# Optimization experiments

Measured on AMD Instinct MI355X. Metric: run time of the kernel, lower is better.

## Reference

```python
import jax, jax.numpy as jnp
import numpy as np

T, B, H = 2048, 32, 1024
L1, L2, L3 = 100, 10, 1  # cascade 100 -> 10 -> 1 from linear_size=100


def setup_inputs() -> dict:
    key = jax.random.key(0)
    ks = jax.random.split(key, 8)
    def lin_init(k, fan_in, shape):
        # torch nn.Linear default: U(-1/sqrt(fan_in), 1/sqrt(fan_in))
        bound = 1.0 / np.sqrt(fan_in)
        return jax.random.uniform(k, shape, jnp.float32, -bound, bound)
    return {
        "encoder_output": jax.random.normal(ks[0], (T, B, H), jnp.float32),
        "lengths": jax.random.randint(ks[1], (B,), 1, T + 1, jnp.int64),
        "W1": lin_init(ks[2], H, (L1, H)),
        "b1": lin_init(ks[3], H, (L1,)),
        "W2": lin_init(ks[4], L1, (L2, L1)),
        "b2": lin_init(ks[5], L1, (L2,)),
        "W3": lin_init(ks[6], L2, (L3, L2)),
        "b3": lin_init(ks[7], L2, (L3,)),
    }


def reference(encoder_output, lengths, W1, b1, W2, b2, W3, b3):
    # MLP cascade over all timesteps/batch at once: [T,B,H] -> [T,B,1]
    h = jax.nn.relu(jnp.einsum("tbh,lh->tbl", encoder_output, W1) + b1)
    h = jax.nn.relu(jnp.einsum("tbl,ml->tbm", h, W2) + b2)
    logits = jnp.einsum("tbm,om->tbo", h, W3) + b3  # [T,B,1]
    logp = jax.nn.log_sigmoid(logits)[..., 0]       # [T,B]
    # Mask timesteps beyond each sample's length, sum, exponentiate
    mask = jnp.arange(T)[:, None] < lengths[None, :]  # [T,B]
    return jnp.exp(jnp.sum(jnp.where(mask, logp, 0.0), axis=0))  # [B]
```

## Files before the change

kernel.cpp:

```cpp
#include <hip/hip_runtime.h>
#include <hip/hip_bf16.h>
#include <stdint.h>


#define T_DIM 2048
#define B_DIM 32
#define H_DIM 1024
#define L1_DIM 100
#define L2_DIM 10
#define K2_PAD 128
#define NPART 512

#define W1B_ELEMS (112 * 1024)
#define W2B_ELEMS (16 * 128)
#define PART_OFF_BYTES ((W1B_ELEMS + W2B_ELEMS) * 2)

#define CHUNK_BYTES 14336
#define LDSH_OFF    0
#define LDSW2_OFF   34816
#define LDSPART_OFF 39168
#define LDS_TOTAL   39680

typedef float v4f __attribute__((ext_vector_type(4)));
typedef short s8  __attribute__((ext_vector_type(8)));

static __device__ __forceinline__ unsigned short f2bf(float f) {
    unsigned int u = __float_as_uint(f);
    u += 0x7fffu + ((u >> 16) & 1u);
    return (unsigned short)(u >> 16);
}

static __device__ __forceinline__ s8 pack8(float4 a, float4 b) {
    union { s8 v; __hip_bfloat162 h[4]; } u;
    u.h[0] = __float22bfloat162_rn(make_float2(a.x, a.y));
    u.h[1] = __float22bfloat162_rn(make_float2(a.z, a.w));
    u.h[2] = __float22bfloat162_rn(make_float2(b.x, b.y));
    u.h[3] = __float22bfloat162_rn(make_float2(b.z, b.w));
    return u.v;
}

__global__ void convert_weights(const float* __restrict__ W1,
                                const float* __restrict__ W2,
                                unsigned short* __restrict__ wsb) {
    int i = blockIdx.x * 256 + threadIdx.x;
    if (i < W1B_ELEMS) {
        int row = i >> 10, col = i & 1023;
        float v = (row < L1_DIM) ? W1[row * H_DIM + col] : 0.0f;
        wsb[i] = f2bf(v);
    } else {
        int j = i - W1B_ELEMS;
        if (j < W2B_ELEMS) {
            int r = j >> 7, c = j & 127;
            float v = (r < L2_DIM && c < L1_DIM) ? W2[r * L1_DIM + c] : 0.0f;
            wsb[W1B_ELEMS + j] = f2bf(v);
        }
    }
}

__global__ __launch_bounds__(256) void mlp_main(
    const float* __restrict__ enc,
    const int*   __restrict__ lenp,
    const float* __restrict__ b1,
    const float* __restrict__ b2,
    const float* __restrict__ W3,
    const float* __restrict__ b3,
    const unsigned short* __restrict__ w1b,
    const unsigned short* __restrict__ w2b,
    float* __restrict__ partials)
{
    __shared__ __align__(16) unsigned char smem[LDS_TOTAL];

    const int tid  = threadIdx.x;
    const int blk  = blockIdx.x;
    const int lane = tid & 63;
    const int w    = tid >> 6;
    const int m    = lane & 15;
    const int q    = lane >> 4;

    const bool is64 = (lenp[1] == 0);

    int maxlen = 0;
    for (int i = 0; i < B_DIM; ++i) {
        int L = is64 ? lenp[2 * i] : lenp[i];
        maxlen = max(maxlen, L);
    }
    if (4 * blk >= maxlen) {
        if (tid < 32) partials[tid * NPART + blk] = 0.0f;
        return;
    }

    const int t = 4 * blk + w;
    const int len0 = is64 ? lenp[2 * m] : lenp[m];
    const int len1 = is64 ? lenp[2 * (16 + m)] : lenp[16 + m];
    const bool pred0 = (t < len0);
    const bool pred1 = (t < len1);
    const bool waveActive = (t < maxlen);

    {
        unsigned short* ldsW2 = (unsigned short*)(smem + LDSW2_OFF);
        int r = tid >> 4, c = (tid & 15) << 3;
        *(uint4*)(ldsW2 + r * 136 + c) = *(const uint4*)(w2b + r * K2_PAD + c);
    }

    float b1v[7];
#pragma unroll
    for (int nt = 0; nt < 7; ++nt) {
        int n = nt * 16 + m;
        b1v[nt] = (n < L1_DIM) ? b1[n] : 0.0f;
    }
    const float b2v = (m < L2_DIM) ? b2[m] : 0.0f;
    const float w3v = (m < L2_DIM) ? W3[m] : 0.0f;
    const float b3s = b3[0];

    const float* ap0 = enc + (size_t)(blk * 128 + w * 32 + m) * H_DIM + q * 8;
    const float* ap1 = ap0 + 16 * H_DIM;
    const int fragoff = lane * 16;

    v4f acc0[7], acc1[7];
#pragma unroll
    for (int nt = 0; nt < 7; ++nt) { acc0[nt] = (v4f)0.0f; acc1[nt] = (v4f)0.0f; }

#define STAGE(kc, BASE)                                                        \
    {                                                                          \
        _Pragma("unroll")                                                      \
        for (int it = 0; it < 4; ++it) {                                       \
            int j = it * 256 + tid;                                            \
            if (it < 3 || tid < 128) {                                         \
                int rest = j >> 6;                           \
                int ks = (rest >= 7) ? 1 : 0;                                  \
                int nt = rest - ks * 7;                                        \
                const unsigned short* g = w1b + (nt * 16 + (j & 15)) * H_DIM + \
                                          (kc) * 64 + ks * 32 + ((j >> 4) & 3) * 8; \
                __builtin_amdgcn_global_load_lds(                              \
                    (const __attribute__((address_space(1))) unsigned int*)g,  \
                    (__attribute__((address_space(3))) unsigned int*)           \
                        (smem + (BASE) + (j & ~63) * 16),                      \
                    16, 0, 0);                                                 \
            }                                                                  \
        }                                                                      \
    }

#define KBODY(kc, RD, WR)                                                      \
    {                                                                          \
        if ((kc) < 15) STAGE((kc) + 1, WR);                                    \
        if (waveActive) {                                                      \
            const int kb = (kc) * 64;                                          \
            const float4 z4 = make_float4(0.f, 0.f, 0.f, 0.f);                 \
            float4 a00 = pred0 ? *(const float4*)(ap0 + kb)      : z4;         \
            float4 a01 = pred0 ? *(const float4*)(ap0 + kb + 4)  : z4;         \
            float4 a02 = pred0 ? *(const float4*)(ap0 + kb + 32) : z4;         \
            float4 a03 = pred0 ? *(const float4*)(ap0 + kb + 36) : z4;         \
            float4 a10 = pred1 ? *(const float4*)(ap1 + kb)      : z4;         \
            float4 a11 = pred1 ? *(const float4*)(ap1 + kb + 4)  : z4;         \
            float4 a12 = pred1 ? *(const float4*)(ap1 + kb + 32) : z4;         \
            float4 a13 = pred1 ? *(const float4*)(ap1 + kb + 36) : z4;         \
            s8 af0 = pack8(a00, a01);                                          \
            s8 af1 = pack8(a10, a11);                                          \
            _Pragma("unroll")                                                  \
            for (int nt = 0; nt < 7; ++nt) {                                   \
                s8 bf = *(const s8*)(smem + (RD) + nt * 1024 + fragoff);       \
                acc0[nt] = __builtin_amdgcn_mfma_f32_16x16x32_bf16(af0, bf, acc0[nt], 0, 0, 0); \
                acc1[nt] = __builtin_amdgcn_mfma_f32_16x16x32_bf16(af1, bf, acc1[nt], 0, 0, 0); \
            }                                                                  \
            af0 = pack8(a02, a03);                                             \
            af1 = pack8(a12, a13);                                             \
            _Pragma("unroll")                                                  \
            for (int nt = 0; nt < 7; ++nt) {                                   \
                s8 bf = *(const s8*)(smem + (RD) + (7 + nt) * 1024 + fragoff); \
                acc0[nt] = __builtin_amdgcn_mfma_f32_16x16x32_bf16(af0, bf, acc0[nt], 0, 0, 0); \
                acc1[nt] = __builtin_amdgcn_mfma_f32_16x16x32_bf16(af1, bf, acc1[nt], 0, 0, 0); \
            }                                                                  \
        }                                                                      \
        __syncthreads();                                                       \
    }

    STAGE(0, 0)
    __syncthreads();

    KBODY(0, 0, CHUNK_BYTES)
    KBODY(1, CHUNK_BYTES, 0)
    KBODY(2, 0, CHUNK_BYTES)
    KBODY(3, CHUNK_BYTES, 0)
    KBODY(4, 0, CHUNK_BYTES)
    KBODY(5, CHUNK_BYTES, 0)
    KBODY(6, 0, CHUNK_BYTES)
    KBODY(7, CHUNK_BYTES, 0)
    KBODY(8, 0, CHUNK_BYTES)
    KBODY(9, CHUNK_BYTES, 0)
    KBODY(10, 0, CHUNK_BYTES)
    KBODY(11, CHUNK_BYTES, 0)
    KBODY(12, 0, CHUNK_BYTES)
    KBODY(13, CHUNK_BYTES, 0)
    KBODY(14, 0, CHUNK_BYTES)
    KBODY(15, CHUNK_BYTES, 0)

#undef KBODY
#undef STAGE

    unsigned short* ldsH = (unsigned short*)(smem + LDSH_OFF);
#pragma unroll
    for (int f = 0; f < 2; ++f) {
#pragma unroll
        for (int nt = 0; nt < 7; ++nt) {
#pragma unroll
            for (int reg = 0; reg < 4; ++reg) {
                int row = w * 32 + f * 16 + q * 4 + reg;
                int col = nt * 16 + m;
                float a = f ? acc1[nt][reg] : acc0[nt][reg];
                ldsH[row * 136 + col] = f2bf(fmaxf(a + b1v[nt], 0.0f));
            }
        }
    }
    {
        int r = tid >> 1, c = 112 + (tid & 1) * 8;
        uint4 z; z.x = z.y = z.z = z.w = 0u;
        *(uint4*)(ldsH + r * 136 + c) = z;
    }
    __syncthreads();

    unsigned short* ldsW2 = (unsigned short*)(smem + LDSW2_OFF);
    v4f acc2[2];
    acc2[0] = (v4f)0.0f; acc2[1] = (v4f)0.0f;
#pragma unroll
    for (int ks2 = 0; ks2 < 4; ++ks2) {
        s8 bw = *(const s8*)(ldsW2 + m * 136 + ks2 * 32 + q * 8);
#pragma unroll
        for (int f = 0; f < 2; ++f) {
            s8 ah = *(const s8*)(ldsH + (w * 32 + f * 16 + m) * 136 + ks2 * 32 + q * 8);
            acc2[f] = __builtin_amdgcn_mfma_f32_16x16x32_bf16(ah, bw, acc2[f], 0, 0, 0);
        }
    }

    float* ldsPart = (float*)(smem + LDSPART_OFF);
#pragma unroll
    for (int f = 0; f < 2; ++f) {
        v4f zv;
#pragma unroll
        for (int reg = 0; reg < 4; ++reg)
            zv[reg] = fmaxf(acc2[f][reg] + b2v, 0.0f) * w3v;
#pragma unroll
        for (int msk = 1; msk < 16; msk <<= 1) {
#pragma unroll
            for (int reg = 0; reg < 4; ++reg)
                zv[reg] += __shfl_xor(zv[reg], msk, 16);
        }
        if (m == 0) {
#pragma unroll
            for (int reg = 0; reg < 4; ++reg) {
                int b = f * 16 + q * 4 + reg;
                int lenB = is64 ? lenp[2 * b] : lenp[b];
                float logit = zv[reg] + b3s;
                float logp  = fminf(logit, 0.0f) - log1pf(__expf(-fabsf(logit)));
                ldsPart[w * 32 + b] = (t < lenB) ? logp : 0.0f;
            }
        }
    }
    __syncthreads();
    if (tid < 32)
        partials[tid * NPART + blk] =
            (ldsPart[tid] + ldsPart[32 + tid]) + (ldsPart[64 + tid] + ldsPart[96 + tid]);
}

__global__ void finalize(const float* __restrict__ partials,
                         float* __restrict__ out) {
    const int b = blockIdx.x;
    const int tid = threadIdx.x;
    float s = 0.0f;
    for (int i = tid; i < NPART; i += 256) s += partials[b * NPART + i];
#pragma unroll
    for (int off = 32; off > 0; off >>= 1) s += __shfl_down(s, off, 64);
    __shared__ float red[4];
    if ((tid & 63) == 0) red[tid >> 6] = s;
    __syncthreads();
    if (tid == 0) out[b] = expf(red[0] + red[1] + red[2] + red[3]);
}

extern "C" void kernel_launch(void* const* d_in, const int* in_sizes, int n_in,
                              void* d_out, int out_size, void* d_ws, size_t ws_size,
                              hipStream_t stream) {
    const float* enc = (const float*)d_in[0];
    const int*   len = (const int*)d_in[1];
    const float* W1  = (const float*)d_in[2];
    const float* b1  = (const float*)d_in[3];
    const float* W2  = (const float*)d_in[4];
    const float* b2  = (const float*)d_in[5];
    const float* W3  = (const float*)d_in[6];
    const float* b3  = (const float*)d_in[7];

    unsigned short* wsb = (unsigned short*)d_ws;
    float* partials = (float*)((char*)d_ws + PART_OFF_BYTES);
    float* out = (float*)d_out;

    convert_weights<<<(W1B_ELEMS + W2B_ELEMS + 255) / 256, 256, 0, stream>>>(W1, W2, wsb);
    mlp_main<<<NPART, 256, 0, stream>>>(enc, len, b1, b2, W3, b3,
                                        wsb, wsb + W1B_ELEMS, partials);
    finalize<<<B_DIM, 256, 0, stream>>>(partials, out);
}
```

Before: 445.9 us.

## Stage activations through LDS with coalesced loads and pre-swizzle W1 fragments

The encoder activation tile is now loaded cooperatively with row-contiguous, coalesced float4 reads, converted to bf16 and written into a double-buffered LDS region in MFMA fragment order. Previously each wave read A fragments straight from global memory in a strided pattern. W1 is also pre-packed by the conversion kernel into fragment order, so staging becomes one linear copy per chunk, and one barrier before the layer-2 step is removed. This raises LDS use to about 67 KB per block, which may cut occupancy, and adds an LDS write/read round trip for A.

```diff
diff --git a/kernel.cpp b/kernel.cpp
--- a/kernel.cpp
+++ b/kernel.cpp
@@ -3,23 +3,23 @@
 #include <stdint.h>
 
 
-#define T_DIM 2048
-#define B_DIM 32
-#define H_DIM 1024
+#define H_DIM  1024
 #define L1_DIM 100
 #define L2_DIM 10
-#define K2_PAD 128
-#define NPART 512
-
-#define W1B_ELEMS (112 * 1024)
-#define W2B_ELEMS (16 * 128)
-#define PART_OFF_BYTES ((W1B_ELEMS + W2B_ELEMS) * 2)
-
-#define CHUNK_BYTES 14336
-#define LDSH_OFF    0
-#define LDSW2_OFF   34816
-#define LDSPART_OFF 39168
-#define LDS_TOTAL   39680
+#define NPART  512
+
+#define W1P_ELEMS (112 * 1024)
+#define W2P_ELEMS (16 * 128)
+#define PART_OFF_BYTES ((W1P_ELEMS + W2P_ELEMS) * 2)
+
+#define W1CH   14336
+#define ACH    16384
+#define W1_OFF 0
+#define A_OFF  28672
+#define H_OFF  28672
+#define W2_OFF 63488
+#define PRT_OFF 67840
+#define LDS_TOTAL 68352
 
 typedef float v4f __attribute__((ext_vector_type(4)));
 typedef short s8  __attribute__((ext_vector_type(8)));
@@ -42,18 +42,31 @@
 __global__ void convert_weights(const float* __restrict__ W1,
                                 const float* __restrict__ W2,
                                 unsigned short* __restrict__ wsb) {
-    int i = blockIdx.x * 256 + threadIdx.x;
-    if (i < W1B_ELEMS) {
-        int row = i >> 10, col = i & 1023;
-        float v = (row < L1_DIM) ? W1[row * H_DIM + col] : 0.0f;
-        wsb[i] = f2bf(v);
-    } else {
-        int j = i - W1B_ELEMS;
-        if (j < W2B_ELEMS) {
-            int r = j >> 7, c = j & 127;
-            float v = (r < L2_DIM && c < L1_DIM) ? W2[r * L1_DIM + c] : 0.0f;
-            wsb[W1B_ELEMS + j] = f2bf(v);
-        }
+    int s = blockIdx.x * 256 + threadIdx.x;
+    union { uint4 u; unsigned short h[8]; } o;
+    if (s < 14336) {
+        int lane = s & 63, rest = s >> 6;
+        int nt = rest % 7, ksc = rest / 7;
+        int m = lane & 15, q = lane >> 4;
+        int row = nt * 16 + m;
+        int col = ksc * 32 + q * 8;
+        if (row < L1_DIM) {
+            const float* src = W1 + row * H_DIM + col;
+#pragma unroll
+            for (int e = 0; e < 8; ++e) o.h[e] = f2bf(src[e]);
+        } else {
+            o.u = make_uint4(0u, 0u, 0u, 0u);
+        }
+        *(uint4*)(wsb + s * 8) = o.u;
+    } else if (s < 14336 + 256) {
+        int j = s - 14336;
+        int r = j >> 4, c = (j & 15) * 8;
+#pragma unroll
+        for (int e = 0; e < 8; ++e) {
+            int cc = c + e;
+            o.h[e] = (r < L2_DIM && cc < L1_DIM) ? f2bf(W2[r * L1_DIM + cc]) : 0;
+        }
+        *(uint4*)(wsb + W1P_ELEMS + j * 8) = o.u;
     }
 }
 
@@ -64,8 +77,8 @@
     const float* __restrict__ b2,
     const float* __restrict__ W3,
     const float* __restrict__ b3,
-    const unsigned short* __restrict__ w1b,
-    const unsigned short* __restrict__ w2b,
+    const unsigned short* __restrict__ w1p,
+    const unsigned short* __restrict__ w2p,
     float* __restrict__ partials)
 {
     __shared__ __align__(16) unsigned char smem[LDS_TOTAL];
@@ -80,7 +93,7 @@
     const bool is64 = (lenp[1] == 0);
 
     int maxlen = 0;
-    for (int i = 0; i < B_DIM; ++i) {
+    for (int i = 0; i < 32; ++i) {
         int L = is64 ? lenp[2 * i] : lenp[i];
         maxlen = max(maxlen, L);
     }
@@ -89,17 +102,22 @@
         return;
     }
 
+    const int srow = tid >> 3;
+    const int scg  = tid & 7;
+    const int sks  = scg >> 2;
+    const int sq   = scg & 3;
+    const int sf   = srow >> 4;
+    const int sm   = srow & 15;
+    const int sslot = sq * 16 + sm;
+    const int slen = is64 ? lenp[2 * srow] : lenp[srow];
+    const float* sp = enc + ((size_t)(blk * 128) + srow) * H_DIM + scg * 8;
+
     const int t = 4 * blk + w;
-    const int len0 = is64 ? lenp[2 * m] : lenp[m];
-    const int len1 = is64 ? lenp[2 * (16 + m)] : lenp[16 + m];
-    const bool pred0 = (t < len0);
-    const bool pred1 = (t < len1);
     const bool waveActive = (t < maxlen);
 
     {
-        unsigned short* ldsW2 = (unsigned short*)(smem + LDSW2_OFF);
-        int r = tid >> 4, c = (tid & 15) << 3;
-        *(uint4*)(ldsW2 + r * 136 + c) = *(const uint4*)(w2b + r * K2_PAD + c);
+        int r = tid >> 4, c = (tid & 15) * 8;
+        *(uint4*)(smem + W2_OFF + r * 272 + c * 2) = *(const uint4*)(w2p + r * 128 + c);
     }
 
     float b1v[7];
@@ -112,92 +130,107 @@
     const float w3v = (m < L2_DIM) ? W3[m] : 0.0f;
     const float b3s = b3[0];
 
-    const float* ap0 = enc + (size_t)(blk * 128 + w * 32 + m) * H_DIM + q * 8;
-    const float* ap1 = ap0 + 16 * H_DIM;
-    const int fragoff = lane * 16;
-
     v4f acc0[7], acc1[7];
 #pragma unroll
     for (int nt = 0; nt < 7; ++nt) { acc0[nt] = (v4f)0.0f; acc1[nt] = (v4f)0.0f; }
 
-#define STAGE(kc, BASE)                                                        \
-    {                                                                          \
-        _Pragma("unroll")                                                      \
-        for (int it = 0; it < 4; ++it) {                                       \
-            int j = it * 256 + tid;                                            \
-            if (it < 3 || tid < 128) {                                         \
-                int rest = j >> 6;                           \
-                int ks = (rest >= 7) ? 1 : 0;                                  \
-                int nt = rest - ks * 7;                                        \
-                const unsigned short* g = w1b + (nt * 16 + (j & 15)) * H_DIM + \
-                                          (kc) * 64 + ks * 32 + ((j >> 4) & 3) * 8; \
-                __builtin_amdgcn_global_load_lds(                              \
-                    (const __attribute__((address_space(1))) unsigned int*)g,  \
-                    (__attribute__((address_space(3))) unsigned int*)           \
-                        (smem + (BASE) + (j & ~63) * 16),                      \
-                    16, 0, 0);                                                 \
-            }                                                                  \
-        }                                                                      \
-    }
-
-#define KBODY(kc, RD, WR)                                                      \
-    {                                                                          \
-        if ((kc) < 15) STAGE((kc) + 1, WR);                                    \
-        if (waveActive) {                                                      \
-            const int kb = (kc) * 64;                                          \
-            const float4 z4 = make_float4(0.f, 0.f, 0.f, 0.f);                 \
-            float4 a00 = pred0 ? *(const float4*)(ap0 + kb)      : z4;         \
-            float4 a01 = pred0 ? *(const float4*)(ap0 + kb + 4)  : z4;         \
-            float4 a02 = pred0 ? *(const float4*)(ap0 + kb + 32) : z4;         \
-            float4 a03 = pred0 ? *(const float4*)(ap0 + kb + 36) : z4;         \
-            float4 a10 = pred1 ? *(const float4*)(ap1 + kb)      : z4;         \
-            float4 a11 = pred1 ? *(const float4*)(ap1 + kb + 4)  : z4;         \
-            float4 a12 = pred1 ? *(const float4*)(ap1 + kb + 32) : z4;         \
-            float4 a13 = pred1 ? *(const float4*)(ap1 + kb + 36) : z4;         \
-            s8 af0 = pack8(a00, a01);                                          \
-            s8 af1 = pack8(a10, a11);                                          \
-            _Pragma("unroll")                                                  \
-            for (int nt = 0; nt < 7; ++nt) {                                   \
-                s8 bf = *(const s8*)(smem + (RD) + nt * 1024 + fragoff);       \
-                acc0[nt] = __builtin_amdgcn_mfma_f32_16x16x32_bf16(af0, bf, acc0[nt], 0, 0, 0); \
-                acc1[nt] = __builtin_amdgcn_mfma_f32_16x16x32_bf16(af1, bf, acc1[nt], 0, 0, 0); \
-            }                                                                  \
-            af0 = pack8(a02, a03);                                             \
-            af1 = pack8(a12, a13);                                             \
-            _Pragma("unroll")                                                  \
-            for (int nt = 0; nt < 7; ++nt) {                                   \
-                s8 bf = *(const s8*)(smem + (RD) + (7 + nt) * 1024 + fragoff); \
-                acc0[nt] = __builtin_amdgcn_mfma_f32_16x16x32_bf16(af0, bf, acc0[nt], 0, 0, 0); \
-                acc1[nt] = __builtin_amdgcn_mfma_f32_16x16x32_bf16(af1, bf, acc1[nt], 0, 0, 0); \
-            }                                                                  \
-        }                                                                      \
-        __syncthreads();                                                       \
-    }
-
-    STAGE(0, 0)
+    const float4 z4c = make_float4(0.f, 0.f, 0.f, 0.f);
+    float4 pa[8];
+
+#define STAGEW(kc, BASE)                                                     \
+    {                                                                        \
+        _Pragma("unroll")                                                    \
+        for (int it = 0; it < 4; ++it) {                                     \
+            int j = it * 256 + tid;                                          \
+            if (it < 3 || tid < 128) {                                       \
+                __builtin_amdgcn_global_load_lds(                            \
+                    (const __attribute__((address_space(1))) unsigned int*)  \
+                        (w1p + (size_t)(kc) * 7168 + j * 8),                 \
+                    (__attribute__((address_space(3))) unsigned int*)        \
+                        (smem + (BASE) + (j & ~63) * 16),                    \
+                    16, 0, 0);                                               \
+            }                                                                \
+        }                                                                    \
+    }
+
+#define LOADA(kc)                                                            \
+    {                                                                        \
+        _Pragma("unroll")                                                    \
+        for (int p = 0; p < 4; ++p) {                                        \
+            bool pr = (4 * blk + p) < slen;                                  \
+            const float* s_ = sp + p * 32768 + (kc) * 64;                    \
+            pa[2 * p]     = pr ? *(const float4*)(s_)     : z4c;             \
+            pa[2 * p + 1] = pr ? *(const float4*)(s_ + 4) : z4c;             \
+        }                                                                    \
+    }
+
+#define WRITEA(BASE)                                                         \
+    {                                                                        \
+        _Pragma("unroll")                                                    \
+        for (int p = 0; p < 4; ++p) {                                        \
+            s8 v_ = pack8(pa[2 * p], pa[2 * p + 1]);                         \
+            *(s8*)(smem + (BASE) + (p * 4 + sf * 2 + sks) * 1024             \
+                   + sslot * 16) = v_;                                       \
+        }                                                                    \
+    }
+
+#define KCOMP(W1RD, ARD)                                                     \
+    if (waveActive) {                                                        \
+        _Pragma("unroll")                                                    \
+        for (int ks = 0; ks < 2; ++ks) {                                     \
+            s8 af0 = *(const s8*)(smem + (ARD) + (w * 4 + ks) * 1024         \
+                                  + lane * 16);                              \
+            s8 af1 = *(const s8*)(smem + (ARD) + (w * 4 + 2 + ks) * 1024     \
+                                  + lane * 16);                              \
+            _Pragma("unroll")                                                \
+            for (int nt = 0; nt < 7; ++nt) {                                 \
+                s8 bf = *(const s8*)(smem + (W1RD)                           \
+                                     + ((ks * 7 + nt) * 64 + lane) * 16);    \
+                acc0[nt] = __builtin_amdgcn_mfma_f32_16x16x32_bf16(          \
+                    af0, bf, acc0[nt], 0, 0, 0);                             \
+                acc1[nt] = __builtin_amdgcn_mfma_f32_16x16x32_bf16(          \
+                    af1, bf, acc1[nt], 0, 0, 0);                             \
+            }                                                                \
+        }                                                                    \
+    }
+
+#define KBODY(kc, W1RD, W1WR, ARD, AWR)                                      \
+    {                                                                        \
+        if ((kc) < 15) { STAGEW((kc) + 1, W1WR); LOADA((kc) + 1); }          \
+        KCOMP(W1RD, ARD);                                                    \
+        if ((kc) < 15) { WRITEA(AWR); }                                      \
+        __syncthreads();                                                     \
+    }
+
+    STAGEW(0, W1_OFF)
+    LOADA(0)
+    WRITEA(A_OFF)
     __syncthreads();
 
-    KBODY(0, 0, CHUNK_BYTES)
-    KBODY(1, CHUNK_BYTES, 0)
-    KBODY(2, 0, CHUNK_BYTES)
-    KBODY(3, CHUNK_BYTES, 0)
-    KBODY(4, 0, CHUNK_BYTES)
-    KBODY(5, CHUNK_BYTES, 0)
-    KBODY(6, 0, CHUNK_BYTES)
-    KBODY(7, CHUNK_BYTES, 0)
-    KBODY(8, 0, CHUNK_BYTES)
-    KBODY(9, CHUNK_BYTES, 0)
-    KBODY(10, 0, CHUNK_BYTES)
-    KBODY(11, CHUNK_BYTES, 0)
-    KBODY(12, 0, CHUNK_BYTES)
-    KBODY(13, CHUNK_BYTES, 0)
-    KBODY(14, 0, CHUNK_BYTES)
-    KBODY(15, CHUNK_BYTES, 0)
+    KBODY(0,  W1_OFF,        W1_OFF + W1CH, A_OFF,       A_OFF + ACH)
+    KBODY(1,  W1_OFF + W1CH, W1_OFF,        A_OFF + ACH, A_OFF)
+    KBODY(2,  W1_OFF,        W1_OFF + W1CH, A_OFF,       A_OFF + ACH)
+    KBODY(3,  W1_OFF + W1CH, W1_OFF,        A_OFF + ACH, A_OFF)
+    KBODY(4,  W1_OFF,        W1_OFF + W1CH, A_OFF,       A_OFF + ACH)
+    KBODY(5,  W1_OFF + W1CH, W1_OFF,        A_OFF + ACH, A_OFF)
+    KBODY(6,  W1_OFF,        W1_OFF + W1CH, A_OFF,       A_OFF + ACH)
+    KBODY(7,  W1_OFF + W1CH, W1_OFF,        A_OFF + ACH, A_OFF)
+    KBODY(8,  W1_OFF,        W1_OFF + W1CH, A_OFF,       A_OFF + ACH)
+    KBODY(9,  W1_OFF + W1CH, W1_OFF,        A_OFF + ACH, A_OFF)
+    KBODY(10, W1_OFF,        W1_OFF + W1CH, A_OFF,       A_OFF + ACH)
+    KBODY(11, W1_OFF + W1CH, W1_OFF,        A_OFF + ACH, A_OFF)
+    KBODY(12, W1_OFF,        W1_OFF + W1CH, A_OFF,       A_OFF + ACH)
+    KBODY(13, W1_OFF + W1CH, W1_OFF,        A_OFF + ACH, A_OFF)
+    KBODY(14, W1_OFF,        W1_OFF + W1CH, A_OFF,       A_OFF + ACH)
+    KBODY(15, W1_OFF + W1CH, W1_OFF,        A_OFF + ACH, A_OFF)
 
 #undef KBODY
-#undef STAGE
-
-    unsigned short* ldsH = (unsigned short*)(smem + LDSH_OFF);
+#undef KCOMP
+#undef WRITEA
+#undef LOADA
+#undef STAGEW
+
+    unsigned short* ldsH = (unsigned short*)(smem + H_OFF);
 #pragma unroll
     for (int f = 0; f < 2; ++f) {
 #pragma unroll
@@ -212,13 +245,13 @@
         }
     }
     {
-        int r = tid >> 1, c = 112 + (tid & 1) * 8;
+        int row = w * 32 + (lane >> 1);
+        int c = 112 + (lane & 1) * 8;
         uint4 z; z.x = z.y = z.z = z.w = 0u;
-        *(uint4*)(ldsH + r * 136 + c) = z;
-    }
-    __syncthreads();
-
-    unsigned short* ldsW2 = (unsigned short*)(smem + LDSW2_OFF);
+        *(uint4*)(ldsH + row * 136 + c) = z;
+    }
+
+    unsigned short* ldsW2 = (unsigned short*)(smem + W2_OFF);
     v4f acc2[2];
     acc2[0] = (v4f)0.0f; acc2[1] = (v4f)0.0f;
 #pragma unroll
@@ -231,7 +264,7 @@
         }
     }
 
-    float* ldsPart = (float*)(smem + LDSPART_OFF);
+    float* ldsPart = (float*)(smem + PRT_OFF);
 #pragma unroll
     for (int f = 0; f < 2; ++f) {
         v4f zv;
@@ -291,8 +324,8 @@
     float* partials = (float*)((char*)d_ws + PART_OFF_BYTES);
     float* out = (float*)d_out;
 
-    convert_weights<<<(W1B_ELEMS + W2B_ELEMS + 255) / 256, 256, 0, stream>>>(W1, W2, wsb);
+    convert_weights<<<57, 256, 0, stream>>>(W1, W2, wsb);
     mlp_main<<<NPART, 256, 0, stream>>>(enc, len, b1, b2, W3, b3,
-                                        wsb, wsb + W1B_ELEMS, partials);
-    finalize<<<B_DIM, 256, 0, stream>>>(partials, out);
-}
+                                        wsb, wsb + W1P_ELEMS, partials);
+    finalize<<<32, 256, 0, stream>>>(partials, out);
+}
```

After: 462.2 us. +3.6%, slower.
